# Optimization experiments

Hardware: AMD Instinct MI355X
Metric: run time of the kernel (lower is better)

## Reference

```python
import jax, jax.numpy as jnp
import numpy as np

VOCAB = 32000
EMBED = 256
H1 = 512          # decoder_hidden_dim (lstm1 hidden)
KV = 128          # key_value_size (lstm2 hidden)


def setup_inputs() -> dict:
    key0 = jax.random.key(0)
    ks = jax.random.split(key0, 12)
    B, S, T = 32, 512, 256
    inp = {}
    inp["key"] = jax.random.normal(ks[0], (B, S, KV), dtype=jnp.float32)
    inp["value"] = jax.random.normal(ks[1], (B, S, KV), dtype=jnp.float32)
    inp["encoder_len"] = jax.random.randint(ks[2], (B,), 1, S + 1)
    inp["y"] = jax.random.randint(ks[3], (B, T), 0, VOCAB)
    # parameters (torch LSTMCell layout: gates ordered i, f, g, o)
    sE = 1.0
    inp["E"] = jax.random.normal(ks[4], (VOCAB, EMBED), dtype=jnp.float32) * sE  # tied embed/output weight
    s1 = 1.0 / np.sqrt(H1)
    inp["W_ih1"] = jax.random.uniform(ks[5], (4 * H1, EMBED), minval=-s1, maxval=s1, dtype=jnp.float32)
    inp["b_ih1"] = jax.random.uniform(ks[6], (4 * H1,), minval=-s1, maxval=s1, dtype=jnp.float32)
    inp["b_hh1"] = jax.random.uniform(ks[7], (4 * H1,), minval=-s1, maxval=s1, dtype=jnp.float32)
    s2 = 1.0 / np.sqrt(KV)
    inp["W_ih2"] = jax.random.uniform(ks[8], (4 * KV, H1), minval=-s2, maxval=s2, dtype=jnp.float32)
    inp["b_ih2"] = jax.random.uniform(ks[9], (4 * KV,), minval=-s2, maxval=s2, dtype=jnp.float32)
    inp["b_hh2"] = jax.random.uniform(ks[10], (4 * KV,), minval=-s2, maxval=s2, dtype=jnp.float32)
    sb = 1.0 / np.sqrt(EMBED)
    inp["b_out"] = jax.random.uniform(ks[11], (VOCAB,), minval=-sb, maxval=sb, dtype=jnp.float32)
    return inp


def _lstm_cell_zero_state(x, W_ih, b_ih, b_hh, H):
    # torch LSTMCell with h_prev = c_prev = 0: W_hh term vanishes, f-gate inert.
    gates = x @ W_ih.T + (b_ih + b_hh)            # (..., 4H)
    i, f, g, o = jnp.split(gates, 4, axis=-1)
    c = jax.nn.sigmoid(i) * jnp.tanh(g)           # c = f*0 + i*g
    return jax.nn.sigmoid(o) * jnp.tanh(c)        # h


def reference(key, value, encoder_len, y, E, W_ih1, b_ih1, b_hh1, W_ih2, b_ih2, b_hh2, b_out):
    B, S, _ = key.shape
    T = y.shape[1]
    # Source loop uses zero LSTM state every step -> timesteps are independent.
    # input at t=0 is the zero-initialized `prediction` long tensor; t>0 uses y[:, t-1].
    inputs = jnp.concatenate([jnp.zeros((B, 1), dtype=y.dtype), y[:, :-1]], axis=1)  # (B, T)
    embed = E[inputs]                                          # (B, T, EMBED)
    h1 = _lstm_cell_zero_state(embed, W_ih1, b_ih1, b_hh1, H1)  # (B, T, H1)
    h2 = _lstm_cell_zero_state(h1, W_ih2, b_ih2, b_hh2, KV)     # (B, T, KV)
    # dot-product attention: energy[b,t,s] = key[b,s,:] . h2[b,t,:]
    energy = jnp.einsum("bsk,btk->bts", key, h2)                # (B, T, S)
    mask = (jnp.arange(S)[None, None, :] >= encoder_len[:, None, None])
    energy = jnp.where(mask, jnp.float32(-1e9), energy)
    attn = jax.nn.softmax(energy, axis=-1)
    context = jnp.einsum("bts,bsv->btv", attn, value)           # (B, T, KV)
    out_ctx = jnp.concatenate([h2, context], axis=-1)           # (B, T, 2*KV == EMBED)
    logits = out_ctx @ E.T + b_out                              # (B, T, VOCAB), tied weights
    return jnp.transpose(logits, (0, 2, 1))                     # (B, VOCAB, T) as in source
```

## Files before the change

kernel.cpp:

```cpp
#include <hip/hip_runtime.h>
#include <stdint.h>

#define VOCAB 32000
#define EMBED 256
#define H1DIM 512
#define KVDIM 128
#define BB    32
#define SS    512
#define TT    256
#define MTOT  (BB*TT)

typedef __attribute__((ext_vector_type(8))) short  short8;
typedef __attribute__((ext_vector_type(4))) float  floatx4;

__device__ __forceinline__ unsigned short f2bf(float f){
  unsigned int x = __float_as_uint(f);
  x += 0x7fffu + ((x >> 16) & 1u);
  return (unsigned short)(x >> 16);
}
__device__ __forceinline__ float sigm(float x){ return 1.0f/(1.0f + __expf(-x)); }

__device__ __forceinline__ void async_lds16(const void* g, void* s){
  typedef const __attribute__((address_space(1))) unsigned int* gp_t;
  typedef __attribute__((address_space(3))) unsigned int* lp_t;
  __builtin_amdgcn_global_load_lds((gp_t)g, (lp_t)s, 16, 0, 0);
}

__global__ __launch_bounds__(256) void cvt_kernel(const float* __restrict__ src,
                                                  unsigned short* __restrict__ dst, int n4){
  int i = blockIdx.x*256 + threadIdx.x;
  if (i >= n4) return;
  float4 v = ((const float4*)src)[i];
  ushort4 o;
  o.x = f2bf(v.x); o.y = f2bf(v.y); o.z = f2bf(v.z); o.w = f2bf(v.w);
  ((ushort4*)dst)[i] = o;
}

template<bool GATHER, int K, int RI, int RG, int RO, int OSTRIDE>
__global__ __launch_bounds__(256) void lstm_gemm_kernel(
    const float* __restrict__ A, const int* __restrict__ y,
    const float* __restrict__ W, const float* __restrict__ b_ih,
    const float* __restrict__ b_hh, float* __restrict__ Hout)
{
  __shared__ __align__(16) float At[32][68];
  __shared__ __align__(16) float Bi[32][68];
  __shared__ __align__(16) float Bg[32][68];
  __shared__ __align__(16) float Bo[32][68];

  const int tid = threadIdx.x;
  const int j0  = blockIdx.x * 64;
  const int m0  = blockIdx.y * 64;

  const int sr  = tid >> 3;
  const int skc = tid & 7;

  const float* arow[2];
  if (GATHER){
    #pragma unroll
    for (int q=0;q<2;q++){
      int m = m0 + sr + q*32;
      int t = m & (TT-1), bb = m >> 8;
      int tok = (t == 0) ? 0 : y[bb*TT + t - 1];
      arow[q] = A + (size_t)tok * K;
    }
  } else {
    arow[0] = A + (size_t)(m0 + sr) * K;
    arow[1] = A + (size_t)(m0 + sr + 32) * K;
  }
  const float* wrow[6];
  wrow[0] = W + (size_t)(RI + j0 + sr) * K;
  wrow[1] = W + (size_t)(RI + j0 + sr + 32) * K;
  wrow[2] = W + (size_t)(RG + j0 + sr) * K;
  wrow[3] = W + (size_t)(RG + j0 + sr + 32) * K;
  wrow[4] = W + (size_t)(RO + j0 + sr) * K;
  wrow[5] = W + (size_t)(RO + j0 + sr + 32) * K;

  float aI[4][4] = {{0}}, aG[4][4] = {{0}}, aO[4][4] = {{0}};
  const int tx = tid & 15, ty = tid >> 4;

  for (int k0 = 0; k0 < K; k0 += 32){
    __syncthreads();
    #pragma unroll
    for (int q=0;q<2;q++){
      int r = sr + q*32;
      float4 va = *(const float4*)(arow[q]   + k0 + skc*4);
      float4 vi = *(const float4*)(wrow[q]   + k0 + skc*4);
      float4 vg = *(const float4*)(wrow[2+q] + k0 + skc*4);
      float4 vo = *(const float4*)(wrow[4+q] + k0 + skc*4);
      At[skc*4+0][r]=va.x; At[skc*4+1][r]=va.y; At[skc*4+2][r]=va.z; At[skc*4+3][r]=va.w;
      Bi[skc*4+0][r]=vi.x; Bi[skc*4+1][r]=vi.y; Bi[skc*4+2][r]=vi.z; Bi[skc*4+3][r]=vi.w;
      Bg[skc*4+0][r]=vg.x; Bg[skc*4+1][r]=vg.y; Bg[skc*4+2][r]=vg.z; Bg[skc*4+3][r]=vg.w;
      Bo[skc*4+0][r]=vo.x; Bo[skc*4+1][r]=vo.y; Bo[skc*4+2][r]=vo.z; Bo[skc*4+3][r]=vo.w;
    }
    __syncthreads();
    #pragma unroll 8
    for (int kk=0;kk<32;kk++){
      float a[4], bi[4], bg[4], bo[4];
      *(float4*)a  = *(const float4*)&At[kk][ty*4];
      *(float4*)bi = *(const float4*)&Bi[kk][tx*4];
      *(float4*)bg = *(const float4*)&Bg[kk][tx*4];
      *(float4*)bo = *(const float4*)&Bo[kk][tx*4];
      #pragma unroll
      for (int mi=0;mi<4;mi++){
        #pragma unroll
        for (int ni=0;ni<4;ni++){
          aI[mi][ni] = fmaf(a[mi], bi[ni], aI[mi][ni]);
          aG[mi][ni] = fmaf(a[mi], bg[ni], aG[mi][ni]);
          aO[mi][ni] = fmaf(a[mi], bo[ni], aO[mi][ni]);
        }
      }
    }
  }
  #pragma unroll
  for (int ni=0;ni<4;ni++){
    int j = j0 + tx*4 + ni;
    float bI = b_ih[RI+j] + b_hh[RI+j];
    float bG = b_ih[RG+j] + b_hh[RG+j];
    float bO = b_ih[RO+j] + b_hh[RO+j];
    #pragma unroll
    for (int mi=0;mi<4;mi++){
      float iv = sigm(aI[mi][ni] + bI);
      float gv = tanhf(aG[mi][ni] + bG);
      float ov = sigm(aO[mi][ni] + bO);
      Hout[(size_t)(m0 + ty*4 + mi) * OSTRIDE + j] = ov * tanhf(iv * gv);
    }
  }
}

__global__ __launch_bounds__(256) void attn_kernel(
    const float* __restrict__ key, const float* __restrict__ value,
    const int* __restrict__ enc_len, const float* __restrict__ h2,
    unsigned short* __restrict__ oc)
{
  __shared__ __align__(16) float h2s[16][128];
  __shared__ __align__(16) float kst[128][36];
  __shared__ __align__(16) float es[16][512];
  __shared__ float red[16][17];
  __shared__ float rmax[16], rsinv[16];

  const int tid = threadIdx.x;
  const int b   = blockIdx.x >> 4;
  const int t0  = (blockIdx.x & 15) * 16;
  const int L   = enc_len[b];

  {
    int r = tid >> 4, c0 = (tid & 15) * 8;
    const float* src = h2 + ((size_t)(b*TT + t0 + r))*KVDIM + c0;
    float4 v0 = *(const float4*)src;
    float4 v1 = *(const float4*)(src + 4);
    *(float4*)&h2s[r][c0]   = v0;
    *(float4*)&h2s[r][c0+4] = v1;
    unsigned short* od = oc + ((size_t)(b*TT + t0 + r))*EMBED + c0;
    od[0]=f2bf(v0.x); od[1]=f2bf(v0.y); od[2]=f2bf(v0.z); od[3]=f2bf(v0.w);
    od[4]=f2bf(v1.x); od[5]=f2bf(v1.y); od[6]=f2bf(v1.z); od[7]=f2bf(v1.w);
  }

  const int ksr = tid >> 3, kcg = tid & 7;
  const int sl  = tid & 31, g = tid >> 5;
  const int tb  = g*2;

  for (int s0 = 0; s0 < SS; s0 += 32){
    __syncthreads();
    {
      const float* kr = key + ((size_t)(b*SS + s0 + ksr))*KVDIM;
      #pragma unroll
      for (int u=0; u<4; u++){
        int c = u*32 + kcg*4;
        float4 kv = *(const float4*)(kr + c);
        kst[c+0][ksr]=kv.x; kst[c+1][ksr]=kv.y; kst[c+2][ksr]=kv.z; kst[c+3][ksr]=kv.w;
      }
    }
    __syncthreads();
    float a0=0.f, a1=0.f;
    #pragma unroll 4
    for (int c=0;c<128;c+=4){
      float k0v=kst[c][sl], k1v=kst[c+1][sl], k2v=kst[c+2][sl], k3v=kst[c+3][sl];
      float4 h0 = *(const float4*)&h2s[tb][c];
      float4 h1 = *(const float4*)&h2s[tb+1][c];
      a0 = fmaf(k0v,h0.x, fmaf(k1v,h0.y, fmaf(k2v,h0.z, fmaf(k3v,h0.w, a0))));
      a1 = fmaf(k0v,h1.x, fmaf(k1v,h1.y, fmaf(k2v,h1.z, fmaf(k3v,h1.w, a1))));
    }
    int s = s0 + sl;
    bool valid = s < L;
    es[tb  ][s] = valid ? a0 : -1e9f;
    es[tb+1][s] = valid ? a1 : -1e9f;
  }
  __syncthreads();

  {
    int row = tid >> 4, l = tid & 15;
    float mx = -3e38f;
    for (int s=l; s<SS; s+=16) mx = fmaxf(mx, es[row][s]);
    red[row][l] = mx;
    __syncthreads();
    if (l == 0){
      float m2 = -3e38f;
      #pragma unroll
      for (int i=0;i<16;i++) m2 = fmaxf(m2, red[row][i]);
      rmax[row] = m2;
    }
    __syncthreads();
    float m = rmax[row], sum = 0.f;
    for (int s=l; s<SS; s+=16){
      float p = __expf(es[row][s] - m);
      es[row][s] = p;
      sum += p;
    }
    red[row][l] = sum;
    __syncthreads();
    if (l == 0){
      float tsum = 0.f;
      #pragma unroll
      for (int i=0;i<16;i++) tsum += red[row][i];
      rsinv[row] = 1.0f / tsum;
    }
    __syncthreads();
  }

  {
    int v = tid & 127, hh = tid >> 7;
    float acc[8] = {0,0,0,0,0,0,0,0};
    const float* vp = value + ((size_t)b*SS)*KVDIM + v;
    #pragma unroll 2
    for (int s=0; s<SS; s+=4){
      float x0 = vp[(size_t)(s+0)*KVDIM];
      float x1 = vp[(size_t)(s+1)*KVDIM];
      float x2 = vp[(size_t)(s+2)*KVDIM];
      float x3 = vp[(size_t)(s+3)*KVDIM];
      #pragma unroll
      for (int i=0;i<8;i++){
        float4 e = *(const float4*)&es[hh*8+i][s];
        acc[i] = fmaf(e.x,x0, fmaf(e.y,x1, fmaf(e.z,x2, fmaf(e.w,x3, acc[i]))));
      }
    }
    #pragma unroll
    for (int i=0;i<8;i++){
      int tt = hh*8 + i;
      oc[((size_t)(b*TT + t0 + tt))*EMBED + KVDIM + v] = f2bf(acc[i] * rsinv[tt]);
    }
  }
}

__global__ __launch_bounds__(256) void out_gemm_kernel(
    const unsigned short* __restrict__ Ebf, const unsigned short* __restrict__ OC,
    const float* __restrict__ b_out, float* __restrict__ out)
{
  __shared__ __align__(16) char smem[16384];
  char* As = smem;
  char* Bs = smem + 8192;

  const int tid  = threadIdx.x;
  const int lane = tid & 63, w = tid >> 6;
  const int v0 = blockIdx.x * 128;
  const int t0 = blockIdx.y * 128;
  const int b  = blockIdx.z;
  const int wv = (w & 1) * 64, wt = (w >> 1) * 64;

  const char* Ab = (const char*)Ebf + (size_t)v0 * (EMBED*2);
  const char* Bb = (const char*)OC  + ((size_t)(b*TT + t0)) * (EMBED*2);

  const int r0 = tid >> 2;
  const int cb = (tid & 3) * 16;
  char* ldsA0 = As        + w * 1024;
  char* ldsA1 = As + 4096 + w * 1024;
  char* ldsB0 = Bs        + w * 1024;
  char* ldsB1 = Bs + 4096 + w * 1024;

  floatx4 zero = {0.f, 0.f, 0.f, 0.f};
  floatx4 acc[4][4];
  #pragma unroll
  for (int i=0;i<4;i++)
    #pragma unroll
    for (int j=0;j<4;j++) acc[i][j] = zero;

  const int fr = lane & 15;
  const int fo = (lane >> 4) * 16;

  for (int kt = 0; kt < 8; kt++){
    const size_t ko = (size_t)kt * 64;
    async_lds16(Ab + (size_t)(r0     )*512 + ko + cb, ldsA0);
    async_lds16(Ab + (size_t)(r0 + 64)*512 + ko + cb, ldsA1);
    async_lds16(Bb + (size_t)(r0     )*512 + ko + cb, ldsB0);
    async_lds16(Bb + (size_t)(r0 + 64)*512 + ko + cb, ldsB1);
    __syncthreads();

    short8 af[4], bq[4];
    #pragma unroll
    for (int i=0;i<4;i++) af[i] = *(const short8*)(As + (wv + i*16 + fr)*64 + fo);
    #pragma unroll
    for (int j=0;j<4;j++) bq[j] = *(const short8*)(Bs + (wt + j*16 + fr)*64 + fo);
    #pragma unroll
    for (int i=0;i<4;i++)
      #pragma unroll
      for (int j=0;j<4;j++)
        acc[i][j] = __builtin_amdgcn_mfma_f32_16x16x32_bf16(af[i], bq[j], acc[i][j], 0, 0, 0);
    __syncthreads();
  }

  const int tc = t0 + wt + fr;
  #pragma unroll
  for (int i=0;i<4;i++){
    int vb = v0 + wv + i*16 + (lane >> 4)*4;
    #pragma unroll
    for (int r=0;r<4;r++){
      int v = vb + r;
      float bo = b_out[v];
      float* orow = out + ((size_t)b*VOCAB + v)*TT + tc;
      #pragma unroll
      for (int j=0;j<4;j++)
        orow[j*16] = acc[i][j][r] + bo;
    }
  }
}

extern "C" void kernel_launch(void* const* d_in, const int* in_sizes, int n_in,
                              void* d_out, int out_size, void* d_ws, size_t ws_size,
                              hipStream_t stream) {
  const float* key   = (const float*)d_in[0];
  const float* value = (const float*)d_in[1];
  const int*   elen  = (const int*)  d_in[2];
  const int*   y     = (const int*)  d_in[3];
  const float* E     = (const float*)d_in[4];
  const float* W1    = (const float*)d_in[5];
  const float* bi1   = (const float*)d_in[6];
  const float* bh1   = (const float*)d_in[7];
  const float* W2    = (const float*)d_in[8];
  const float* bi2   = (const float*)d_in[9];
  const float* bh2   = (const float*)d_in[10];
  const float* bo    = (const float*)d_in[11];
  float* out = (float*)d_out;

  char* ws = (char*)d_ws;
  float*          h1  = (float*)ws;
  float*          h2  = (float*)(ws + 16777216);
  unsigned short* Ebf = (unsigned short*)(ws + 20971520);
  unsigned short* OC  = (unsigned short*)(ws + 37355520);

  cvt_kernel<<<8000, 256, 0, stream>>>(E, Ebf, (VOCAB*EMBED)/4);
  lstm_gemm_kernel<true, 256, 0, 1024, 1536, 512>
      <<<dim3(8, 128), 256, 0, stream>>>(E, y, W1, bi1, bh1, h1);
  lstm_gemm_kernel<false, 512, 0, 256, 384, 128>
      <<<dim3(2, 128), 256, 0, stream>>>(h1, nullptr, W2, bi2, bh2, h2);
  attn_kernel<<<512, 256, 0, stream>>>(key, value, elen, h2, OC);
  out_gemm_kernel<<<dim3(VOCAB/128, TT/128, BB), 256, 0, stream>>>(Ebf, OC, bo, out);
}
```

Measured before the change: 1.453 ms.

## Move LSTM GEMMs to fp16 MFMA with pre-gathered embeddings and swizzled output grid

Replaces the fp32 FMA LSTM gate GEMMs with fp16 MFMA kernels fed by async global-to-LDS loads. The embedding gather and the weight conversions to fp16 now run in separate kernels, and h1 is stored as fp16. The output GEMM grid is flattened and remapped so consecutive blocks share vocabulary tiles, which should improve L2 reuse of E. Fast-math sigmoid and tanh replace the library calls. The cost is reduced precision in the LSTM path and a few extra small launches.

```diff
diff --git a/kernel.cpp b/kernel.cpp
--- a/kernel.cpp
+++ b/kernel.cpp
@@ -10,15 +10,21 @@
 #define TT    256
 #define MTOT  (BB*TT)
 
-typedef __attribute__((ext_vector_type(8))) short  short8;
-typedef __attribute__((ext_vector_type(4))) float  floatx4;
+typedef __attribute__((ext_vector_type(8))) short    short8;
+typedef __attribute__((ext_vector_type(4))) float    floatx4;
+typedef __attribute__((ext_vector_type(8))) _Float16 half8;
+typedef __attribute__((ext_vector_type(4))) _Float16 half4;
 
 __device__ __forceinline__ unsigned short f2bf(float f){
   unsigned int x = __float_as_uint(f);
   x += 0x7fffu + ((x >> 16) & 1u);
   return (unsigned short)(x >> 16);
 }
-__device__ __forceinline__ float sigm(float x){ return 1.0f/(1.0f + __expf(-x)); }
+__device__ __forceinline__ float sigm(float x){ return __fdividef(1.0f, 1.0f + __expf(-x)); }
+__device__ __forceinline__ float ftanh(float x){
+  float e = __expf(2.0f*x);
+  return 1.0f - __fdividef(2.0f, e + 1.0f);
+}
 
 __device__ __forceinline__ void async_lds16(const void* g, void* s){
   typedef const __attribute__((address_space(1))) unsigned int* gp_t;
@@ -36,93 +42,126 @@
   ((ushort4*)dst)[i] = o;
 }
 
-template<bool GATHER, int K, int RI, int RG, int RO, int OSTRIDE>
-__global__ __launch_bounds__(256) void lstm_gemm_kernel(
-    const float* __restrict__ A, const int* __restrict__ y,
-    const float* __restrict__ W, const float* __restrict__ b_ih,
-    const float* __restrict__ b_hh, float* __restrict__ Hout)
+__global__ __launch_bounds__(256) void cvt16_kernel(const float* __restrict__ src,
+                                                    _Float16* __restrict__ dst, int n4){
+  int i = blockIdx.x*256 + threadIdx.x;
+  if (i >= n4) return;
+  float4 v = ((const float4*)src)[i];
+  half4 o;
+  o[0] = (_Float16)v.x; o[1] = (_Float16)v.y; o[2] = (_Float16)v.z; o[3] = (_Float16)v.w;
+  ((half4*)dst)[i] = o;
+}
+
+__global__ __launch_bounds__(256) void gather16_kernel(const float* __restrict__ E,
+    const int* __restrict__ y, _Float16* __restrict__ out){
+  int g = blockIdx.x*256 + threadIdx.x;
+  int m = g >> 5;
+  int e = (g & 31) * 8;
+  int t = m & (TT-1), bb = m >> 8;
+  int tok = (t == 0) ? 0 : y[bb*TT + t - 1];
+  const float* src = E + (size_t)tok*EMBED + e;
+  float4 v0 = *(const float4*)src;
+  float4 v1 = *(const float4*)(src + 4);
+  half8 h;
+  h[0]=(_Float16)v0.x; h[1]=(_Float16)v0.y; h[2]=(_Float16)v0.z; h[3]=(_Float16)v0.w;
+  h[4]=(_Float16)v1.x; h[5]=(_Float16)v1.y; h[6]=(_Float16)v1.z; h[7]=(_Float16)v1.w;
+  *(half8*)(out + (size_t)m*EMBED + e) = h;
+}
+
+template<int K, int RI, int RG, int RO, int OSTRIDE, bool OF16>
+__global__ __launch_bounds__(256) void lstm_mfma_kernel(
+    const _Float16* __restrict__ A16, const _Float16* __restrict__ W16,
+    const float* __restrict__ b_ih, const float* __restrict__ b_hh,
+    void* __restrict__ Hout)
 {
-  __shared__ __align__(16) float At[32][68];
-  __shared__ __align__(16) float Bi[32][68];
-  __shared__ __align__(16) float Bg[32][68];
-  __shared__ __align__(16) float Bo[32][68];
-
-  const int tid = threadIdx.x;
-  const int j0  = blockIdx.x * 64;
-  const int m0  = blockIdx.y * 64;
-
-  const int sr  = tid >> 3;
-  const int skc = tid & 7;
-
-  const float* arow[2];
-  if (GATHER){
-    #pragma unroll
-    for (int q=0;q<2;q++){
-      int m = m0 + sr + q*32;
-      int t = m & (TT-1), bb = m >> 8;
-      int tok = (t == 0) ? 0 : y[bb*TT + t - 1];
-      arow[q] = A + (size_t)tok * K;
-    }
-  } else {
-    arow[0] = A + (size_t)(m0 + sr) * K;
-    arow[1] = A + (size_t)(m0 + sr + 32) * K;
-  }
-  const float* wrow[6];
-  wrow[0] = W + (size_t)(RI + j0 + sr) * K;
-  wrow[1] = W + (size_t)(RI + j0 + sr + 32) * K;
-  wrow[2] = W + (size_t)(RG + j0 + sr) * K;
-  wrow[3] = W + (size_t)(RG + j0 + sr + 32) * K;
-  wrow[4] = W + (size_t)(RO + j0 + sr) * K;
-  wrow[5] = W + (size_t)(RO + j0 + sr + 32) * K;
-
-  float aI[4][4] = {{0}}, aG[4][4] = {{0}}, aO[4][4] = {{0}};
-  const int tx = tid & 15, ty = tid >> 4;
-
-  for (int k0 = 0; k0 < K; k0 += 32){
-    __syncthreads();
-    #pragma unroll
-    for (int q=0;q<2;q++){
-      int r = sr + q*32;
-      float4 va = *(const float4*)(arow[q]   + k0 + skc*4);
-      float4 vi = *(const float4*)(wrow[q]   + k0 + skc*4);
-      float4 vg = *(const float4*)(wrow[2+q] + k0 + skc*4);
-      float4 vo = *(const float4*)(wrow[4+q] + k0 + skc*4);
-      At[skc*4+0][r]=va.x; At[skc*4+1][r]=va.y; At[skc*4+2][r]=va.z; At[skc*4+3][r]=va.w;
-      Bi[skc*4+0][r]=vi.x; Bi[skc*4+1][r]=vi.y; Bi[skc*4+2][r]=vi.z; Bi[skc*4+3][r]=vi.w;
-      Bg[skc*4+0][r]=vg.x; Bg[skc*4+1][r]=vg.y; Bg[skc*4+2][r]=vg.z; Bg[skc*4+3][r]=vg.w;
-      Bo[skc*4+0][r]=vo.x; Bo[skc*4+1][r]=vo.y; Bo[skc*4+2][r]=vo.z; Bo[skc*4+3][r]=vo.w;
-    }
-    __syncthreads();
-    #pragma unroll 8
-    for (int kk=0;kk<32;kk++){
-      float a[4], bi[4], bg[4], bo[4];
-      *(float4*)a  = *(const float4*)&At[kk][ty*4];
-      *(float4*)bi = *(const float4*)&Bi[kk][tx*4];
-      *(float4*)bg = *(const float4*)&Bg[kk][tx*4];
-      *(float4*)bo = *(const float4*)&Bo[kk][tx*4];
-      #pragma unroll
-      for (int mi=0;mi<4;mi++){
+  __shared__ __align__(16) char smem[20480];
+  char* As = smem;
+  char* Bs = smem + 8192;
+
+  const int tid  = threadIdx.x;
+  const int lane = tid & 63, w = tid >> 6;
+  const int j0 = blockIdx.x * 64;
+  const int m0 = blockIdx.y * 128;
+
+  const int r0 = tid >> 2;
+  const int cb = (tid & 3) * 16;
+
+  const char* asrc0 = (const char*)A16 + (size_t)(m0 + r0     ) * (K*2);
+  const char* asrc1 = (const char*)A16 + (size_t)(m0 + r0 + 64) * (K*2);
+  const char* bsrc0 = (const char*)W16 + (size_t)(RI + j0 + r0) * (K*2);
+  const char* bsrc1 = (const char*)W16 + (size_t)(RG + j0 + r0) * (K*2);
+  const char* bsrc2 = (const char*)W16 + (size_t)(RO + j0 + r0) * (K*2);
+
+  char* ldsA0 = As        + w*1024;
+  char* ldsA1 = As + 4096 + w*1024;
+  char* ldsB0 = Bs        + w*1024;
+  char* ldsB1 = Bs + 4096 + w*1024;
+  char* ldsB2 = Bs + 8192 + w*1024;
+
+  const int wv = (w & 1) * 64;
+  const int wj = (w >> 1) * 32;
+
+  floatx4 zero = {0.f,0.f,0.f,0.f};
+  floatx4 acc[4][2][3];
+  #pragma unroll
+  for (int a=0;a<4;a++)
+    #pragma unroll
+    for (int b=0;b<2;b++)
+      #pragma unroll
+      for (int g=0;g<3;g++) acc[a][b][g] = zero;
+
+  const int fr = lane & 15;
+  const int fo = (lane >> 4) * 16;
+
+  for (int kt = 0; kt < K/32; kt++){
+    const int ko = kt*64 + cb;
+    async_lds16(asrc0 + ko, ldsA0);
+    async_lds16(asrc1 + ko, ldsA1);
+    async_lds16(bsrc0 + ko, ldsB0);
+    async_lds16(bsrc1 + ko, ldsB1);
+    async_lds16(bsrc2 + ko, ldsB2);
+    __syncthreads();
+
+    half8 af[4], bfr[2][3];
+    #pragma unroll
+    for (int i=0;i<4;i++)
+      af[i] = *(const half8*)(As + (wv + i*16 + fr)*64 + fo);
+    #pragma unroll
+    for (int ji=0;ji<2;ji++)
+      #pragma unroll
+      for (int g=0;g<3;g++)
+        bfr[ji][g] = *(const half8*)(Bs + g*4096 + (wj + ji*16 + fr)*64 + fo);
+    #pragma unroll
+    for (int mi=0;mi<4;mi++)
+      #pragma unroll
+      for (int ji=0;ji<2;ji++)
         #pragma unroll
-        for (int ni=0;ni<4;ni++){
-          aI[mi][ni] = fmaf(a[mi], bi[ni], aI[mi][ni]);
-          aG[mi][ni] = fmaf(a[mi], bg[ni], aG[mi][ni]);
-          aO[mi][ni] = fmaf(a[mi], bo[ni], aO[mi][ni]);
-        }
+        for (int g=0;g<3;g++)
+          acc[mi][ji][g] = __builtin_amdgcn_mfma_f32_16x16x32_f16(
+              af[mi], bfr[ji][g], acc[mi][ji][g], 0, 0, 0);
+    __syncthreads();
+  }
+
+  #pragma unroll
+  for (int ji=0;ji<2;ji++){
+    const int j = j0 + wj + ji*16 + fr;
+    const float bI = b_ih[RI+j] + b_hh[RI+j];
+    const float bG = b_ih[RG+j] + b_hh[RG+j];
+    const float bO = b_ih[RO+j] + b_hh[RO+j];
+    #pragma unroll
+    for (int mi=0;mi<4;mi++){
+      const int mb = m0 + wv + mi*16 + (lane>>4)*4;
+      #pragma unroll
+      for (int r=0;r<4;r++){
+        float iv = sigm(acc[mi][ji][0][r] + bI);
+        float gv = ftanh(acc[mi][ji][1][r] + bG);
+        float ov = sigm(acc[mi][ji][2][r] + bO);
+        float h  = ov * ftanh(iv * gv);
+        if constexpr (OF16)
+          ((_Float16*)Hout)[(size_t)(mb + r)*OSTRIDE + j] = (_Float16)h;
+        else
+          ((float*)Hout)[(size_t)(mb + r)*OSTRIDE + j] = h;
       }
-    }
-  }
-  #pragma unroll
-  for (int ni=0;ni<4;ni++){
-    int j = j0 + tx*4 + ni;
-    float bI = b_ih[RI+j] + b_hh[RI+j];
-    float bG = b_ih[RG+j] + b_hh[RG+j];
-    float bO = b_ih[RO+j] + b_hh[RO+j];
-    #pragma unroll
-    for (int mi=0;mi<4;mi++){
-      float iv = sigm(aI[mi][ni] + bI);
-      float gv = tanhf(aG[mi][ni] + bG);
-      float ov = sigm(aO[mi][ni] + bO);
-      Hout[(size_t)(m0 + ty*4 + mi) * OSTRIDE + j] = ov * tanhf(iv * gv);
     }
   }
 }
@@ -251,9 +290,16 @@
 
   const int tid  = threadIdx.x;
   const int lane = tid & 63, w = tid >> 6;
-  const int v0 = blockIdx.x * 128;
-  const int t0 = blockIdx.y * 128;
-  const int b  = blockIdx.z;
+
+  const int id     = blockIdx.x;
+  const int chunk  = id >> 9;
+  const int within = id & 511;
+  const int vt = (chunk << 3) + (within >> 6);
+  const int tb = within & 63;
+  const int v0 = vt * 128;
+  const int t0 = (tb & 1) * 128;
+  const int b  = tb >> 1;
+
   const int wv = (w & 1) * 64, wt = (w >> 1) * 64;
 
   const char* Ab = (const char*)Ebf + (size_t)v0 * (EMBED*2);
@@ -331,16 +377,22 @@
   float* out = (float*)d_out;
 
   char* ws = (char*)d_ws;
-  float*          h1  = (float*)ws;
-  float*          h2  = (float*)(ws + 16777216);
-  unsigned short* Ebf = (unsigned short*)(ws + 20971520);
-  unsigned short* OC  = (unsigned short*)(ws + 37355520);
-
-  cvt_kernel<<<8000, 256, 0, stream>>>(E, Ebf, (VOCAB*EMBED)/4);
-  lstm_gemm_kernel<true, 256, 0, 1024, 1536, 512>
-      <<<dim3(8, 128), 256, 0, stream>>>(E, y, W1, bi1, bh1, h1);
-  lstm_gemm_kernel<false, 512, 0, 256, 384, 128>
-      <<<dim3(2, 128), 256, 0, stream>>>(h1, nullptr, W2, bi2, bh2, h2);
+  _Float16*       h1f   = (_Float16*)ws;
+  _Float16*       W1f   = (_Float16*)(ws + 8388608);
+  _Float16*       W2f   = (_Float16*)(ws + 9437184);
+  _Float16*       Emb16 = (_Float16*)(ws + 9961472);
+  float*          h2    = (float*)(ws + 16777216);
+  unsigned short* Ebf   = (unsigned short*)(ws + 20971520);
+  unsigned short* OC    = (unsigned short*)(ws + 37355520);
+
+  cvt_kernel  <<<8000, 256, 0, stream>>>(E,  Ebf, (VOCAB*EMBED)/4);
+  cvt16_kernel<<< 512, 256, 0, stream>>>(W1, W1f, (4*H1DIM*EMBED)/4);
+  cvt16_kernel<<< 256, 256, 0, stream>>>(W2, W2f, (4*KVDIM*H1DIM)/4);
+  gather16_kernel<<<1024, 256, 0, stream>>>(E, y, Emb16);
+  lstm_mfma_kernel<256, 0, 1024, 1536, 512, true>
+      <<<dim3(8, 64), 256, 0, stream>>>(Emb16, W1f, bi1, bh1, h1f);
+  lstm_mfma_kernel<512, 0, 256, 384, 128, false>
+      <<<dim3(2, 64), 256, 0, stream>>>(h1f, W2f, bi2, bh2, h2);
   attn_kernel<<<512, 256, 0, stream>>>(key, value, elen, h2, OC);
-  out_gemm_kernel<<<dim3(VOCAB/128, TT/128, BB), 256, 0, stream>>>(Ebf, OC, bo, out);
-}
+  out_gemm_kernel<<<16000, 256, 0, stream>>>(Ebf, OC, bo, out);
+}
```

Measured after the change: 1.308 ms. 1.11x faster.
